# Optimization experiments

Measured on AMD Instinct MI355X. Metric: run time of the kernel, lower is better.

## Reference

```python
import jax, jax.numpy as jnp
import numpy as np

N_NODE, N_NET, E = 100000, 20000, 200000
H_NODE, H_NET, H_PIN = 64, 32, 16
O_NODE, O_NET = 32, 64


def setup_inputs() -> dict:
    key = jax.random.key(0)
    ks = jax.random.split(key, 8)
    return {
        'node_feat': jax.random.normal(ks[0], (N_NODE, H_NODE), jnp.float32),
        'net_feat': jax.random.normal(ks[1], (N_NET, H_NET), jnp.float32),
        'pin_feat': jax.random.normal(ks[2], (E, H_PIN), jnp.float32),
        'edge_node': jax.random.randint(ks[3], (E,), 0, N_NODE, jnp.int32),
        'edge_net': jax.random.randint(ks[4], (E,), 0, N_NET, jnp.int32),
        'W1': jax.random.normal(ks[5], (H_NODE, O_NET), jnp.float32) * 0.05,
        'b1': jnp.zeros((O_NET,), jnp.float32),
        'W2': jax.random.normal(ks[6], (H_PIN, H_NET * O_NODE), jnp.float32) * 0.05,
        'b2': jnp.zeros((H_NET * O_NODE,), jnp.float32),
        'b_nn': jnp.zeros((O_NODE,), jnp.float32),
    }


def reference(node_feat, net_feat, pin_feat, edge_node, edge_net, W1, b1, W2, b2, b_nn):
    ones = jnp.ones((E,), node_feat.dtype)
    # ---- relation 'pins': node -> net, DGL GraphConv with norm='both' ----
    out_deg = jnp.clip(jax.ops.segment_sum(ones, edge_node, num_segments=N_NODE), 1.0)  # src out-degree
    in_deg = jnp.clip(jax.ops.segment_sum(ones, edge_net, num_segments=N_NET), 1.0)     # dst in-degree
    src = node_feat * jax.lax.rsqrt(out_deg)[:, None]                                   # [N_node, H_node]
    agg = jax.ops.segment_sum(src[edge_node], edge_net, num_segments=N_NET)             # [N_net, H_node]
    net_out = (agg * jax.lax.rsqrt(in_deg)[:, None]) @ W1 + b1                           # [N_net, O_net]
    # ---- relation 'pinned': net -> node, DGL NNConv (mean aggregator) ----
    We = (pin_feat @ W2 + b2).reshape(E, H_NET, O_NODE)                                  # per-edge weight matrix
    msg = jnp.einsum('ei,eio->eo', net_feat[edge_net], We)                               # [E, O_node]
    node_deg = jnp.clip(jax.ops.segment_sum(ones, edge_node, num_segments=N_NODE), 1.0)
    node_out = jax.ops.segment_sum(msg, edge_node, num_segments=N_NODE) / node_deg[:, None] + b_nn
    return node_out, net_out
```

## Files before the change

kernel.cpp:

```cpp
#include <hip/hip_runtime.h>
#include <hip/hip_bf16.h>

#define N_NODE 100000
#define N_NET  20000
#define NE     200000
#define H_NODE 64
#define H_NET  32
#define H_PIN  16
#define O_NODE 32
#define O_NET  64
#define CSR_STRIDE 64


#define OFF_NETCNT  400000
#define OFF_CSR     480000
#define OFF_Z       10720000
#define OFF_C       31200000
#define ZERO_BYTES  480000

static __device__ __forceinline__ unsigned short f2bf(float f) {
    unsigned int u = __float_as_uint(f);
    u += 0x7fff + ((u >> 16) & 1);
    return (unsigned short)(u >> 16);
}
static __device__ __forceinline__ float bf2f(unsigned short h) {
    return __uint_as_float(((unsigned int)h) << 16);
}

#define BLD_EDGE_BLKS 782
#define BLD_Z_BLKS    1250
#define BLD_INIT_BLKS 3125
#define ZNPB 16

__global__ void k_build(const int* __restrict__ en, const int* __restrict__ em,
                        int* __restrict__ node_deg, int* __restrict__ net_cnt,
                        int2* __restrict__ csr,
                        const float* __restrict__ net_feat,
                        const float* __restrict__ W2, const float* __restrict__ b2,
                        unsigned short* __restrict__ Zb, float* __restrict__ C,
                        const float* __restrict__ b_nn,
                        float* __restrict__ out_node) {
    int t = threadIdx.x, b = blockIdx.x;
    if (b < BLD_EDGE_BLKS) {
        int e = b * 256 + t;
        if (e < NE) {
            int v = en[e], n = em[e];
            atomicAdd(&node_deg[v], 1);
            int slot = atomicAdd(&net_cnt[n], 1);
            if (slot < CSR_STRIDE) csr[n * CSR_STRIDE + slot] = make_int2(e, v);
        }
        return;
    }
    if (b < BLD_EDGE_BLKS + BLD_Z_BLKS) {
        __shared__ float sy[ZNPB][H_NET];
        int base = (b - BLD_EDGE_BLKS) * ZNPB;
        for (int idx = t; idx < ZNPB * H_NET; idx += 256)
            sy[idx >> 5][idx & 31] = net_feat[(base + (idx >> 5)) * H_NET + (idx & 31)];
        __syncthreads();
        int o = t & 31, k4 = (t >> 5) & 3, rep = t >> 7;
        const float* w2p = W2 + (k4 * 4) * 1024 + o;
        float4 acc[8];
#pragma unroll
        for (int g = 0; g < 8; g++) acc[g] = make_float4(0.f, 0.f, 0.f, 0.f);
#pragma unroll 4
        for (int i = 0; i < H_NET; i++) {
            float w0 = w2p[0 * 1024 + i * 32];
            float w1 = w2p[1 * 1024 + i * 32];
            float w2v = w2p[2 * 1024 + i * 32];
            float w3 = w2p[3 * 1024 + i * 32];
#pragma unroll
            for (int g = 0; g < 8; g++) {
                float y = sy[rep * 8 + g][i];
                acc[g].x += w0 * y; acc[g].y += w1 * y;
                acc[g].z += w2v * y; acc[g].w += w3 * y;
            }
        }
#pragma unroll
        for (int g = 0; g < 8; g++) {
            int n = base + rep * 8 + g;
            ushort4 uz;
            uz.x = f2bf(acc[g].x); uz.y = f2bf(acc[g].y);
            uz.z = f2bf(acc[g].z); uz.w = f2bf(acc[g].w);
            *(ushort4*)&Zb[(size_t)n * 512 + o * 16 + k4 * 4] = uz;
        }
#pragma unroll
        for (int r = 0; r < 2; r++) {
            int idx = t + r * 256;
            int g = idx >> 5, oo = idx & 31;
            float a = 0.f;
#pragma unroll
            for (int i = 0; i < H_NET; i++) a += sy[g][i] * b2[i * 32 + oo];
            C[(base + g) * 32 + oo] = a;
        }
        return;
    }
    int idx = (b - BLD_EDGE_BLKS - BLD_Z_BLKS) * 256 + t;
    ((float4*)out_node)[idx] = ((const float4*)b_nn)[idx & 7];
}

__global__ void k_net(const float* __restrict__ node_feat,
                      const int* __restrict__ node_deg,
                      const int* __restrict__ net_cnt,
                      const int2* __restrict__ csr,
                      const float* __restrict__ W1,
                      const float* __restrict__ b1,
                      const unsigned short* __restrict__ Zb,
                      const float* __restrict__ Cg,
                      const float* __restrict__ pin_feat,
                      float* __restrict__ out_net, float* __restrict__ out_node) {
    __shared__ float  spin[32][16];
    __shared__ float4 srow4[16];
    int l = threadIdx.x;
    int n = blockIdx.x;
    int beg = n * CSR_STRIDE, deg = net_cnt[n];
    int o = l & 31;
    int half = l >> 5;
    int q = l >> 4, f = l & 15;

    float z[16];
    {
        const uint4* zp = (const uint4*)&Zb[(size_t)n * 512 + o * 16];
        uint4 za = zp[0], zb = zp[1];
        unsigned int uu[8] = {za.x, za.y, za.z, za.w, zb.x, zb.y, zb.z, zb.w};
#pragma unroll
        for (int i = 0; i < 8; i++) {
            z[2 * i]     = bf2f((unsigned short)(uu[i] & 0xffffu));
            z[2 * i + 1] = bf2f((unsigned short)(uu[i] >> 16));
        }
    }
    float c = Cg[n * 32 + o];

    const float4* nf4 = (const float4*)node_feat;
    const float4* pf4 = (const float4*)pin_feat;

    float4 acc4 = make_float4(0.f, 0.f, 0.f, 0.f);

    for (int j0 = 0; j0 < deg; j0 += 32) {
        int cnt = deg - j0; if (cnt > 32) cnt = 32;
        int vj = 0, ej = 0; float sj = 0.f;
        if (l < cnt) {
            int2 ev = csr[beg + j0 + l];
            ej = ev.x; vj = ev.y;
            float dv = (float)node_deg[vj]; if (dv < 1.f) dv = 1.f;
            sj = rsqrtf(dv);
        }
        {
            int jj = l >> 2;
            int src = (jj < cnt) ? jj : cnt - 1;
            int e = __shfl(ej, src);
            float4 pv = pf4[(size_t)e * 4 + (l & 3)];
            ((float4*)&spin[jj][0])[l & 3] = pv;
        }
        if (cnt > 16) {
            int jj = 16 + (l >> 2);
            int src = (jj < cnt) ? jj : cnt - 1;
            int e = __shfl(ej, src);
            float4 pv = pf4[(size_t)e * 4 + (l & 3)];
            ((float4*)&spin[jj][0])[l & 3] = pv;
        }
        {
            int vv[4]; float ss[4];
#pragma unroll
            for (int r = 0; r < 4; r++) {
                int jj = r * 4 + q;
                int src = (jj < cnt) ? jj : cnt - 1;
                vv[r] = __shfl(vj, src);
                float sv = __shfl(sj, src);
                ss[r] = (jj < cnt) ? sv : 0.f;
            }
            float4 xx[4];
#pragma unroll
            for (int r = 0; r < 4; r++) xx[r] = nf4[(size_t)vv[r] * 16 + f];
#pragma unroll
            for (int r = 0; r < 4; r++) {
                acc4.x += xx[r].x * ss[r]; acc4.y += xx[r].y * ss[r];
                acc4.z += xx[r].z * ss[r]; acc4.w += xx[r].w * ss[r];
            }
        }
        if (cnt > 16) {
            int vv[4]; float ss[4];
#pragma unroll
            for (int r = 0; r < 4; r++) {
                int jj = 16 + r * 4 + q;
                int src = (jj < cnt) ? jj : cnt - 1;
                vv[r] = __shfl(vj, src);
                float sv = __shfl(sj, src);
                ss[r] = (jj < cnt) ? sv : 0.f;
            }
            float4 xx[4];
#pragma unroll
            for (int r = 0; r < 4; r++) xx[r] = nf4[(size_t)vv[r] * 16 + f];
#pragma unroll
            for (int r = 0; r < 4; r++) {
                acc4.x += xx[r].x * ss[r]; acc4.y += xx[r].y * ss[r];
                acc4.z += xx[r].z * ss[r]; acc4.w += xx[r].w * ss[r];
            }
        }
        for (int jj = 0; jj < cnt; jj += 2) {
            int je = jj + half;
            int src = (je < cnt) ? je : cnt - 1;
            int v = __shfl(vj, src);
            float sv = __shfl(sj, src);
            float inv = sv * sv;
            const float4* pr = (const float4*)&spin[src][0];
            float m = c;
#pragma unroll
            for (int k4 = 0; k4 < 4; k4++) {
                float4 pv = pr[k4];
                m += pv.x * z[k4 * 4 + 0] + pv.y * z[k4 * 4 + 1]
                   + pv.z * z[k4 * 4 + 2] + pv.w * z[k4 * 4 + 3];
            }
            if (je < cnt) atomicAdd(&out_node[(size_t)v * O_NODE + o], m * inv);
        }
    }
    acc4.x += __shfl_xor(acc4.x, 16); acc4.y += __shfl_xor(acc4.y, 16);
    acc4.z += __shfl_xor(acc4.z, 16); acc4.w += __shfl_xor(acc4.w, 16);
    acc4.x += __shfl_xor(acc4.x, 32); acc4.y += __shfl_xor(acc4.y, 32);
    acc4.z += __shfl_xor(acc4.z, 32); acc4.w += __shfl_xor(acc4.w, 32);
    float dn = (deg < 1) ? 1.f : (float)deg;
    float rs = rsqrtf(dn);
    if (l < 16)
        srow4[l] = make_float4(acc4.x * rs, acc4.y * rs, acc4.z * rs, acc4.w * rs);
    __syncthreads();
    {
        const float* a = (const float*)&srow4[0];
        float oacc = b1[l];
#pragma unroll 16
        for (int h = 0; h < H_NODE; h++) oacc += a[h] * W1[h * O_NET + l];
        out_net[n * O_NET + l] = oacc;
    }
}

extern "C" void kernel_launch(void* const* d_in, const int* in_sizes, int n_in,
                              void* d_out, int out_size, void* d_ws, size_t ws_size,
                              hipStream_t stream) {
    const float* node_feat = (const float*)d_in[0];
    const float* net_feat  = (const float*)d_in[1];
    const float* pin_feat  = (const float*)d_in[2];
    const int*   edge_node = (const int*)d_in[3];
    const int*   edge_net  = (const int*)d_in[4];
    const float* W1        = (const float*)d_in[5];
    const float* b1        = (const float*)d_in[6];
    const float* W2        = (const float*)d_in[7];
    const float* b2        = (const float*)d_in[8];
    const float* b_nn      = (const float*)d_in[9];

    float* out_node = (float*)d_out;
    float* out_net  = out_node + (size_t)N_NODE * O_NODE;

    char* ws = (char*)d_ws;
    int*            node_deg = (int*)ws;
    int*            net_cnt  = (int*)(ws + OFF_NETCNT);
    int2*           csr      = (int2*)(ws + OFF_CSR);
    unsigned short* Zb       = (unsigned short*)(ws + OFF_Z);
    float*          C        = (float*)(ws + OFF_C);

    (void)hipMemsetAsync(ws, 0, ZERO_BYTES, stream);

    k_build<<<BLD_EDGE_BLKS + BLD_Z_BLKS + BLD_INIT_BLKS, 256, 0, stream>>>(
        edge_node, edge_net, node_deg, net_cnt, csr,
        net_feat, W2, b2, Zb, C, b_nn, out_node);

    k_net<<<N_NET, 64, 0, stream>>>(
        node_feat, node_deg, net_cnt, csr,
        W1, b1, Zb, C, pin_feat, out_net, out_node);
}
```

Measured before the change: 160.1 us.

## Build net CSR via per-block LDS histograms, column scan, and deterministic scatter

Replaces the global-atomic CSR slot assignment with a three-pass build. Per-block shared-memory histograms pack two 16-bit net counts per int, a column-wise prefix scan over the 250 blocks gives each block a base offset, and a scatter pass assigns slots with LDS atomics. This removes contended global atomics on net_cnt and makes slot order deterministic. In exchange it adds two kernel launches, 40 MB of histogram traffic, and a serial scan over 250 blocks that runs on only 40 blocks.

```diff
diff --git a/kernel.cpp b/kernel.cpp
--- a/kernel.cpp
+++ b/kernel.cpp
@@ -11,11 +11,18 @@
 #define O_NET  64
 #define CSR_STRIDE 64
 
+#define CNT_BLOCKS    250
+#define EDGES_PER_BLK 800
+#define HIST_STRIDE   10000
+#define SCN_BLKS      40
+
 
 #define OFF_NETCNT  400000
 #define OFF_CSR     480000
 #define OFF_Z       10720000
 #define OFF_C       31200000
+#define OFF_HIST    33760000
+#define OFF_GBASE   43760000
 #define ZERO_BYTES  480000
 
 static __device__ __forceinline__ unsigned short f2bf(float f) {
@@ -27,33 +34,51 @@
     return __uint_as_float(((unsigned int)h) << 16);
 }
 
-#define BLD_EDGE_BLKS 782
-#define BLD_Z_BLKS    1250
-#define BLD_INIT_BLKS 3125
+__global__ void k_count(const int* __restrict__ en, const int* __restrict__ em,
+                        int* __restrict__ node_deg, int* __restrict__ hist) {
+    __shared__ int h[HIST_STRIDE];
+    int t = threadIdx.x, b = blockIdx.x;
+    for (int i = t; i < HIST_STRIDE; i += 256) h[i] = 0;
+    __syncthreads();
+    int e0 = b * EDGES_PER_BLK;
+    for (int k = t; k < EDGES_PER_BLK; k += 256) {
+        int e = e0 + k;
+        int n = em[e];
+        atomicAdd(&h[n >> 1], 1 << ((n & 1) * 16));
+        atomicAdd(&node_deg[en[e]], 1);
+    }
+    __syncthreads();
+    for (int i = t; i < HIST_STRIDE; i += 256) hist[b * HIST_STRIDE + i] = h[i];
+}
+
 #define ZNPB 16
-
-__global__ void k_build(const int* __restrict__ en, const int* __restrict__ em,
-                        int* __restrict__ node_deg, int* __restrict__ net_cnt,
-                        int2* __restrict__ csr,
-                        const float* __restrict__ net_feat,
-                        const float* __restrict__ W2, const float* __restrict__ b2,
-                        unsigned short* __restrict__ Zb, float* __restrict__ C,
-                        const float* __restrict__ b_nn,
-                        float* __restrict__ out_node) {
+#define DNS_Z_BLKS    1250
+#define DNS_INIT_BLKS 3125
+
+__global__ void k_scan_dense(const int* __restrict__ hist, int* __restrict__ gbase,
+                             int* __restrict__ net_cnt,
+                             const float* __restrict__ net_feat,
+                             const float* __restrict__ W2, const float* __restrict__ b2,
+                             unsigned short* __restrict__ Zb, float* __restrict__ C,
+                             const float* __restrict__ b_nn,
+                             float* __restrict__ out_node) {
     int t = threadIdx.x, b = blockIdx.x;
-    if (b < BLD_EDGE_BLKS) {
-        int e = b * 256 + t;
-        if (e < NE) {
-            int v = en[e], n = em[e];
-            atomicAdd(&node_deg[v], 1);
-            int slot = atomicAdd(&net_cnt[n], 1);
-            if (slot < CSR_STRIDE) csr[n * CSR_STRIDE + slot] = make_int2(e, v);
-        }
+    if (b < SCN_BLKS) {
+        int i = b * 256 + t;
+        if (i >= HIST_STRIDE) return;
+        int s0 = 0, s1 = 0;
+#pragma unroll 5
+        for (int bb = 0; bb < CNT_BLOCKS; bb++) {
+            int u = hist[bb * HIST_STRIDE + i];
+            gbase[bb * HIST_STRIDE + i] = (s0 & 0xffff) | (s1 << 16);
+            s0 += u & 0xffff; s1 += (u >> 16) & 0xffff;
+        }
+        ((int2*)net_cnt)[i] = make_int2(s0, s1);
         return;
     }
-    if (b < BLD_EDGE_BLKS + BLD_Z_BLKS) {
+    if (b < SCN_BLKS + DNS_Z_BLKS) {
         __shared__ float sy[ZNPB][H_NET];
-        int base = (b - BLD_EDGE_BLKS) * ZNPB;
+        int base = (b - SCN_BLKS) * ZNPB;
         for (int idx = t; idx < ZNPB * H_NET; idx += 256)
             sy[idx >> 5][idx & 31] = net_feat[(base + (idx >> 5)) * H_NET + (idx & 31)];
         __syncthreads();
@@ -94,8 +119,24 @@
         }
         return;
     }
-    int idx = (b - BLD_EDGE_BLKS - BLD_Z_BLKS) * 256 + t;
+    int idx = (b - SCN_BLKS - DNS_Z_BLKS) * 256 + t;
     ((float4*)out_node)[idx] = ((const float4*)b_nn)[idx & 7];
+}
+
+__global__ void k_scatter(const int* __restrict__ en, const int* __restrict__ em,
+                          const int* __restrict__ gbase, int2* __restrict__ csr) {
+    __shared__ int h[HIST_STRIDE];
+    int t = threadIdx.x, b = blockIdx.x;
+    for (int i = t; i < HIST_STRIDE; i += 256) h[i] = gbase[b * HIST_STRIDE + i];
+    __syncthreads();
+    int e0 = b * EDGES_PER_BLK;
+    for (int k = t; k < EDGES_PER_BLK; k += 256) {
+        int e = e0 + k;
+        int n = em[e], v = en[e];
+        int sh = (n & 1) * 16;
+        int slot = (atomicAdd(&h[n >> 1], 1 << sh) >> sh) & 0xffff;
+        if (slot < CSR_STRIDE) csr[n * CSR_STRIDE + slot] = make_int2(e, v);
+    }
 }
 
 __global__ void k_net(const float* __restrict__ node_feat,
@@ -254,12 +295,17 @@
     int2*           csr      = (int2*)(ws + OFF_CSR);
     unsigned short* Zb       = (unsigned short*)(ws + OFF_Z);
     float*          C        = (float*)(ws + OFF_C);
+    int*            hist     = (int*)(ws + OFF_HIST);
+    int*            gbase    = (int*)(ws + OFF_GBASE);
 
     (void)hipMemsetAsync(ws, 0, ZERO_BYTES, stream);
 
-    k_build<<<BLD_EDGE_BLKS + BLD_Z_BLKS + BLD_INIT_BLKS, 256, 0, stream>>>(
-        edge_node, edge_net, node_deg, net_cnt, csr,
-        net_feat, W2, b2, Zb, C, b_nn, out_node);
+    k_count<<<CNT_BLOCKS, 256, 0, stream>>>(edge_node, edge_net, node_deg, hist);
+
+    k_scan_dense<<<SCN_BLKS + DNS_Z_BLKS + DNS_INIT_BLKS, 256, 0, stream>>>(
+        hist, gbase, net_cnt, net_feat, W2, b2, Zb, C, b_nn, out_node);
+
+    k_scatter<<<CNT_BLOCKS, 256, 0, stream>>>(edge_node, edge_net, gbase, csr);
 
     k_net<<<N_NET, 64, 0, stream>>>(
         node_feat, node_deg, net_cnt, csr,
```

New measurement: 169.8 us. 1.06x slower.
